# Kernel tuning notes

Measured on AMD Instinct MI355X. Metric: run time of the kernel, lower is better.

The kernel has to match this reference:

```python
import jax, jax.numpy as jnp
import numpy as np

HID = 2048
HEAD = 64
NH = HID // HEAD  # 32 heads
B, T = 4, 2048


def setup_inputs() -> dict:
    key = jax.random.key(0)
    ks = jax.random.split(key, 32)
    def n(i, shape, sc):
        return (jax.random.normal(ks[i], shape, jnp.float32) * sc).astype(jnp.float32)
    return {
        "hidden": n(0, (B, T, HID), 1.0),
        "attn_x": n(1, (B, HID), 1.0),
        "attn_kv": n(2, (B, NH, HEAD, HEAD), 0.1),
        "ffn_x": n(3, (B, HID), 1.0),
        "time_maa_x": n(4, (1, 1, HID), 0.5),
        "time_maa_w": n(5, (1, 1, HID), 0.5),
        "time_maa_k": n(6, (1, 1, HID), 0.5),
        "time_maa_v": n(7, (1, 1, HID), 0.5),
        "time_maa_r": n(8, (1, 1, HID), 0.5),
        "time_maa_g": n(9, (1, 1, HID), 0.5),
        "time_maa_w1": n(10, (HID, 160), 0.02),
        "time_maa_w2": n(11, (5, 32, HID), 0.02),
        "time_decay": n(12, (1, 1, HID), 0.5),
        "time_decay_w1": n(13, (HID, 64), 0.02),
        "time_decay_w2": n(14, (64, HID), 0.02),
        "time_faaaa": n(15, (NH, HEAD), 0.5),
        "receptance_w": n(16, (HID, HID), 0.02),
        "key_w": n(17, (HID, HID), 0.02),
        "value_w": n(18, (HID, HID), 0.02),
        "gate_w": n(19, (HID, HID), 0.02),
        "output_w": n(20, (HID, HID), 0.02),
        "gn_gamma": 1.0 + n(21, (HID,), 0.1),
        "gn_beta": n(22, (HID,), 0.1),
    }


def reference(hidden, attn_x, attn_kv, ffn_x,
              time_maa_x, time_maa_w, time_maa_k, time_maa_v, time_maa_r, time_maa_g,
              time_maa_w1, time_maa_w2, time_decay, time_decay_w1, time_decay_w2,
              time_faaaa, receptance_w, key_w, value_w, gate_w, output_w,
              gn_gamma, gn_beta):
    Bb, Tt, C = hidden.shape
    x = hidden
    shifted = jnp.concatenate([attn_x[:, None, :], x[:, :-1, :]], axis=1)
    dx = shifted - x
    time_mix = x + dx * time_maa_x
    # token-shift LoRA: (B,T,C)@(C,160) -> (5,B*T,32)@(5,32,C) -> five mixes
    xxx = jnp.tanh(time_mix @ time_maa_w1).reshape(Bb * Tt, 5, 32).transpose(1, 0, 2)
    xxx = jnp.einsum('nbk,nkc->nbc', xxx, time_maa_w2)
    mw, mk, mv, mr, mg = xxx.reshape(5, Bb, Tt, C)
    xw = x + dx * (time_maa_w + mw)
    xk = x + dx * (time_maa_k + mk)
    xv = x + dx * (time_maa_v + mv)
    xr = x + dx * (time_maa_r + mr)
    xg = x + dx * (time_maa_g + mg)
    r = (xr @ receptance_w).reshape(Bb, Tt, NH, HEAD).transpose(0, 2, 1, 3)  # (B,H,T,hs)
    k = (xk @ key_w).reshape(Bb, Tt, NH, HEAD).transpose(0, 2, 1, 3)
    v = (xv @ value_w).reshape(Bb, Tt, NH, HEAD).transpose(0, 2, 1, 3)
    g = jax.nn.silu(xg @ gate_w)
    td = time_decay + jnp.tanh(xw @ time_decay_w1) @ time_decay_w2  # (B,T,C)
    w = jnp.exp(-jnp.exp(td)).reshape(Bb, Tt, NH, HEAD).transpose(0, 2, 1, 3)
    # Source updates layer_state only AFTER the time loop, so inside the loop the
    # state is the constant attn_kv:  out_t = r_t @ (u * (k_t v_t^T) + S0).
    rk = jnp.einsum('bhtd,hd,bhtd->bht', r, time_faaaa, k)
    out = rk[..., None] * v + jnp.einsum('bhtd,bhde->bhte', r, attn_kv)  # (B,H,T,hs)
    new_attn_kv = k[:, :, -1, :, None] * v[:, :, -1, None, :] + w[:, :, -1, :, None] * attn_kv
    new_attn_x = hidden[:, -1]
    out = out.transpose(0, 2, 1, 3).reshape(Bb, Tt, C)
    # keras GroupNormalization(groups=NH) on (B,T,C): stats over (T, within-group channels)
    go = out.reshape(Bb, Tt, NH, HEAD)
    mean = go.mean(axis=(1, 3), keepdims=True)
    var = go.var(axis=(1, 3), keepdims=True)
    eps = 1e-5 * HEAD ** 2
    out = ((go - mean) * jax.lax.rsqrt(var + eps)).reshape(Bb, Tt, C) * gn_gamma + gn_beta
    out = (out * g) @ output_w
    return out, new_attn_x, new_attn_kv, ffn_x
```

## Files before the change

kernel.cpp:

```cpp
#include <hip/hip_runtime.h>

#define HID 2048
#define TSEQ 2048
#define BBATCH 4
#define MROWS 8192
#define NHEADS 32

typedef float fvec4 __attribute__((ext_vector_type(4)));
typedef unsigned short usvec4 __attribute__((ext_vector_type(4)));
typedef unsigned short usvec8 __attribute__((ext_vector_type(8)));
typedef __bf16 bh8 __attribute__((ext_vector_type(8)));
typedef float f32x4 __attribute__((ext_vector_type(4)));

__device__ __forceinline__ float bf2f(unsigned short u){
  return __uint_as_float(((unsigned int)u) << 16);
}
__device__ __forceinline__ unsigned short f2bf(float f){
  unsigned int u = __float_as_uint(f);
  return (unsigned short)((u + 0x7fffu + ((u >> 16) & 1u)) >> 16);
}
__device__ __forceinline__ void gll16(const void* g, void* lds){
  __builtin_amdgcn_global_load_lds(
      (const __attribute__((address_space(1))) unsigned int*)g,
      (__attribute__((address_space(3))) unsigned int*)lds, 16, 0, 0);
}

__global__ void tcast_kernel(const float* __restrict__ in, unsigned short* __restrict__ out,
                             int R, int C){
  __shared__ float tile[32][33];
  int c0 = blockIdx.x * 32, r0 = blockIdx.y * 32;
  int tx = threadIdx.x, ty = threadIdx.y;
  for (int i = ty; i < 32; i += 8){
    int r = r0 + i, c = c0 + tx;
    tile[i][tx] = (r < R && c < C) ? in[(size_t)r * C + c] : 0.f;
  }
  __syncthreads();
  for (int i = ty; i < 32; i += 8){
    int c = c0 + i, r = r0 + tx;
    if (c < C && r < R) out[(size_t)c * R + r] = f2bf(tile[tx][i]);
  }
}

__global__ void zero_stats_kernel(float* __restrict__ gsum, float* __restrict__ gsqs){
  int i = threadIdx.x;
  gsum[i] = 0.f;
  gsqs[i] = 0.f;
}

__global__ void tmix_kernel(const float* __restrict__ hidden, const float* __restrict__ attn_x,
                            const float* __restrict__ tmx, unsigned short* __restrict__ tm){
  int i4 = blockIdx.x * 256 + threadIdx.x;
  int row = i4 >> 9;
  int c4 = i4 & 511;
  fvec4 x = *(const fvec4*)&hidden[(size_t)i4 * 4];
  fvec4 p;
  if ((row & (TSEQ - 1)) == 0){
    int b = row >> 11;
    p = *(const fvec4*)&attn_x[b * HID + c4 * 4];
  } else {
    p = *(const fvec4*)&hidden[(size_t)(i4 - 512) * 4];
  }
  fvec4 tx = *(const fvec4*)&tmx[c4 * 4];
  fvec4 t = x + (p - x) * tx;
  usvec4 o;
  o[0]=f2bf(t[0]); o[1]=f2bf(t[1]); o[2]=f2bf(t[2]); o[3]=f2bf(t[3]);
  *(usvec4*)&tm[(size_t)i4 * 4] = o;
}

template<int ACT, int OUTBF16>
__global__ __launch_bounds__(256, 2) void gemm_kernel(
    const unsigned short* __restrict__ A, const unsigned short* __restrict__ Bt,
    void* __restrict__ Cptr, int M, int N, int K, int ldc)
{
  __shared__ unsigned short As[128 * 32];
  __shared__ unsigned short Bs[128 * 32];
  const int tid = threadIdx.x;
  const int lane = tid & 63;
  const int w = tid >> 6;
  const int wr = w >> 1, wc = w & 1;
  const int lr = lane & 15, lq = lane >> 4;
  const int rowBase = blockIdx.y * 128;
  const int colBase = blockIdx.x * 128;

  const int arow = tid >> 2;
  const int ach = tid & 3;
  const unsigned short* aptr0 = A + (size_t)(rowBase + arow) * K + ach * 8;
  const unsigned short* aptr1 = aptr0 + (size_t)64 * K;
  int br0 = colBase + arow;      if (br0 > N - 1) br0 = N - 1;
  int br1 = colBase + arow + 64; if (br1 > N - 1) br1 = N - 1;
  const unsigned short* bptr0 = Bt + (size_t)br0 * K + ach * 8;
  const unsigned short* bptr1 = Bt + (size_t)br1 * K + ach * 8;

  f32x4 acc[4][4] = {};

  const int nk = K >> 5;
  for (int kk = 0; kk < nk; ++kk){
    gll16(aptr0, &As[tid * 8]);
    gll16(aptr1, &As[(tid + 256) * 8]);
    gll16(bptr0, &Bs[tid * 8]);
    gll16(bptr1, &Bs[(tid + 256) * 8]);
    aptr0 += 32; aptr1 += 32; bptr0 += 32; bptr1 += 32;
    __syncthreads();
    bh8 af[4], bfv[4];
    #pragma unroll
    for (int m = 0; m < 4; ++m)
      af[m] = *reinterpret_cast<const bh8*>(&As[(wr * 64 + m * 16 + lr) * 32 + lq * 8]);
    #pragma unroll
    for (int n = 0; n < 4; ++n)
      bfv[n] = *reinterpret_cast<const bh8*>(&Bs[(wc * 64 + n * 16 + lr) * 32 + lq * 8]);
    #pragma unroll
    for (int m = 0; m < 4; ++m)
      #pragma unroll
      for (int n = 0; n < 4; ++n)
        acc[m][n] = __builtin_amdgcn_mfma_f32_16x16x32_bf16(af[m], bfv[n], acc[m][n], 0, 0, 0);
    __syncthreads();
  }

  #pragma unroll
  for (int m = 0; m < 4; ++m){
    int gr0 = rowBase + wr * 64 + m * 16 + lq * 4;
    #pragma unroll
    for (int n = 0; n < 4; ++n){
      int gc = colBase + wc * 64 + n * 16 + lr;
      if (gc < N){
        #pragma unroll
        for (int q = 0; q < 4; ++q){
          float v = acc[m][n][q];
          if constexpr (ACT == 1) v = tanhf(v);
          else if constexpr (ACT == 2) v = v / (1.0f + __expf(-v));
          size_t off = (size_t)(gr0 + q) * ldc + gc;
          if constexpr (OUTBF16) ((unsigned short*)Cptr)[off] = f2bf(v);
          else                   ((float*)Cptr)[off] = v;
        }
      }
    }
  }
}

__global__ __launch_bounds__(256) void mix_kernel(
    const float* __restrict__ xxx, const float* __restrict__ hidden,
    const float* __restrict__ attn_x, const float* __restrict__ w2,
    const float* __restrict__ tmk, const float* __restrict__ tmv,
    const float* __restrict__ tmr, const float* __restrict__ tmg,
    unsigned short* __restrict__ xk, unsigned short* __restrict__ xv,
    unsigned short* __restrict__ xr, unsigned short* __restrict__ xg)
{
  __shared__ __attribute__((aligned(16))) unsigned short smem[20992];
  unsigned short* xs   = smem;
  unsigned short* w2t  = smem + 10752;
  unsigned short* out4 = smem;

  const int tid = threadIdx.x;
  const int r0 = blockIdx.y * 64, c0 = blockIdx.x * 64;
  const int w = tid >> 6, lane = tid & 63, lr = lane & 15, lq = lane >> 4;

  for (int idx = tid; idx < 64 * 40; idx += 256){
    int r = idx / 40, cq = idx - r * 40;
    fvec4 v = *(const fvec4*)&xxx[(size_t)(r0 + r) * 160 + cq * 4];
    usvec4 o;
    o[0]=f2bf(v[0]); o[1]=f2bf(v[1]); o[2]=f2bf(v[2]); o[3]=f2bf(v[3]);
    *(usvec4*)&xs[r * 168 + cq * 4] = o;
  }
  for (int idx = tid; idx < 4 * 32 * 16; idx += 256){
    int n = idx >> 9;
    int rem = idx & 511;
    int j = rem >> 4, cq = rem & 15;
    fvec4 v = *(const fvec4*)&w2[(size_t)((n + 1) * 32 + j) * HID + c0 + cq * 4];
    #pragma unroll
    for (int cc = 0; cc < 4; ++cc)
      w2t[(n * 64 + cq * 4 + cc) * 40 + j] = f2bf(v[cc]);
  }
  __syncthreads();

  f32x4 acc[4][4] = {};
  #pragma unroll
  for (int n = 0; n < 4; ++n){
    bh8 afr = *reinterpret_cast<const bh8*>(&xs[(w * 16 + lr) * 168 + (n + 1) * 32 + lq * 8]);
    #pragma unroll
    for (int ct = 0; ct < 4; ++ct){
      bh8 bfr = *reinterpret_cast<const bh8*>(&w2t[(n * 64 + ct * 16 + lr) * 40 + lq * 8]);
      acc[ct][n] = __builtin_amdgcn_mfma_f32_16x16x32_bf16(afr, bfr, acc[ct][n], 0, 0, 0);
    }
  }
  __syncthreads();

  #pragma unroll
  for (int ct = 0; ct < 4; ++ct){
    int gc = c0 + ct * 16 + lr;
    float tk_ = tmk[gc], tv_ = tmv[gc], tr_ = tmr[gc], tg_ = tmg[gc];
    #pragma unroll
    for (int q = 0; q < 4; ++q){
      int row64 = w * 16 + lq * 4 + q;
      int gr = r0 + row64;
      size_t rowoff = (size_t)gr * HID + gc;
      float xx = hidden[rowoff];
      float pp = ((gr & (TSEQ - 1)) == 0) ? attn_x[(gr >> 11) * HID + gc]
                                          : hidden[rowoff - HID];
      float dxv = pp - xx;
      int lo = row64 * 72 + ct * 16 + lr;
      out4[(0 * 64 * 72) + lo] = f2bf(xx + dxv * (tk_ + acc[ct][0][q]));
      out4[(1 * 64 * 72) + lo] = f2bf(xx + dxv * (tv_ + acc[ct][1][q]));
      out4[(2 * 64 * 72) + lo] = f2bf(xx + dxv * (tr_ + acc[ct][2][q]));
      out4[(3 * 64 * 72) + lo] = f2bf(xx + dxv * (tg_ + acc[ct][3][q]));
    }
  }
  __syncthreads();

  #pragma unroll
  for (int a = 0; a < 4; ++a){
    unsigned short* dst = (a == 0) ? xk : (a == 1) ? xv : (a == 2) ? xr : xg;
    #pragma unroll
    for (int pass = 0; pass < 2; ++pass){
      int row64 = pass * 32 + (tid >> 3);
      int c8 = (tid & 7) * 8;
      usvec8 v8 = *(const usvec8*)&out4[(a * 64 + row64) * 72 + c8];
      *(usvec8*)&dst[(size_t)(r0 + row64) * HID + c0 + c8] = v8;
    }
  }
}

__global__ __launch_bounds__(256) void attn_kernel(
    const unsigned short* __restrict__ rb, const unsigned short* __restrict__ kb,
    const unsigned short* __restrict__ vb, const float* __restrict__ attn_kv,
    const float* __restrict__ faaaa, unsigned short* __restrict__ out0b,
    float* __restrict__ gsum, float* __restrict__ gsqs)
{
  const int bh = blockIdx.y;
  const int b = bh >> 5, h = bh & 31;
  const int tid = threadIdx.x, lane = tid & 63, w = tid >> 6;
  const int lr = lane & 15, lq = lane >> 4;
  const int t0 = blockIdx.x * 256 + w * 64;
  const size_t rowbase = (size_t)(b * TSEQ + t0) * HID + h * 64;

  const float* akvp = attn_kv + (size_t)bh * 4096;
  bh8 bfr[2][4];
  #pragma unroll
  for (int kk = 0; kk < 2; ++kk)
    #pragma unroll
    for (int n = 0; n < 4; ++n)
      #pragma unroll
      for (int j = 0; j < 8; ++j)
        bfr[kk][n][j] = (__bf16)akvp[(kk * 32 + lq * 8 + j) * 64 + n * 16 + lr];

  float fa0[8], fa1[8];
  #pragma unroll
  for (int j = 0; j < 8; ++j){
    fa0[j] = faaaa[h * 64 + lq * 8 + j];
    fa1[j] = faaaa[h * 64 + 32 + lq * 8 + j];
  }

  __shared__ __attribute__((aligned(16))) float rk_s[4][64];
  __shared__ __attribute__((aligned(16))) unsigned short outb[4][64][72];

  f32x4 acc[4][4] = {};
  #pragma unroll
  for (int m = 0; m < 4; ++m){
    size_t ra = rowbase + (size_t)(m * 16 + lr) * HID;
    bh8 a0 = *reinterpret_cast<const bh8*>(&rb[ra + lq * 8]);
    bh8 a1 = *reinterpret_cast<const bh8*>(&rb[ra + 32 + lq * 8]);
    usvec8 k0 = *reinterpret_cast<const usvec8*>(&kb[ra + lq * 8]);
    usvec8 k1 = *reinterpret_cast<const usvec8*>(&kb[ra + 32 + lq * 8]);
    float p = 0.f;
    #pragma unroll
    for (int j = 0; j < 8; ++j){
      p += (float)a0[j] * fa0[j] * bf2f(k0[j]);
      p += (float)a1[j] * fa1[j] * bf2f(k1[j]);
    }
    p += __shfl_xor(p, 16, 64);
    p += __shfl_xor(p, 32, 64);
    if (lq == 0) rk_s[w][m * 16 + lr] = p;
    #pragma unroll
    for (int n = 0; n < 4; ++n){
      acc[m][n] = __builtin_amdgcn_mfma_f32_16x16x32_bf16(a0, bfr[0][n], acc[m][n], 0, 0, 0);
      acc[m][n] = __builtin_amdgcn_mfma_f32_16x16x32_bf16(a1, bfr[1][n], acc[m][n], 0, 0, 0);
    }
  }
  __syncthreads();

  float ssum = 0.f, ssq = 0.f;
  #pragma unroll
  for (int m = 0; m < 4; ++m){
    fvec4 rk4 = *(const fvec4*)&rk_s[w][m * 16 + lq * 4];
    #pragma unroll
    for (int n = 0; n < 4; ++n){
      int col = n * 16 + lr;
      #pragma unroll
      for (int q = 0; q < 4; ++q){
        int row = m * 16 + lq * 4 + q;
        float vv = bf2f(vb[rowbase + (size_t)row * HID + col]);
        float o = acc[m][n][q] + rk4[q] * vv;
        ssum += o; ssq += o * o;
        outb[w][row][col] = f2bf(o);
      }
    }
  }
  __syncthreads();
  #pragma unroll
  for (int pass = 0; pass < 8; ++pass){
    int row = pass * 8 + (lane >> 3);
    int c8 = (lane & 7) * 8;
    usvec8 o8 = *(const usvec8*)&outb[w][row][c8];
    *(usvec8*)&out0b[rowbase + (size_t)row * HID + c8] = o8;
  }
  #pragma unroll
  for (int off2 = 32; off2 > 0; off2 >>= 1){
    ssum += __shfl_xor(ssum, off2, 64);
    ssq  += __shfl_xor(ssq,  off2, 64);
  }
  if (lane == 0){ atomicAdd(&gsum[bh], ssum); atomicAdd(&gsqs[bh], ssq); }
}

__global__ void gn_stats_kernel(const float* __restrict__ gsum, const float* __restrict__ gsqs,
                                float* __restrict__ meaninv){
  int g = threadIdx.x;
  const float n = (float)(TSEQ * 64);
  float mean = gsum[g] / n;
  float var = gsqs[g] / n - mean * mean;
  meaninv[2 * g]     = mean;
  meaninv[2 * g + 1] = rsqrtf(var + 1e-5f * 64.0f * 64.0f);
}

__global__ void ynorm_kernel(const unsigned short* __restrict__ out0b,
                             const unsigned short* __restrict__ gb,
                             const float* __restrict__ meaninv, const float* __restrict__ gamma,
                             const float* __restrict__ beta, unsigned short* __restrict__ yb){
  int i4 = blockIdx.x * 256 + threadIdx.x;
  int row = i4 >> 9, c4 = i4 & 511;
  int b = row >> 11;
  int c = c4 * 4;
  int g = b * 32 + (c >> 6);
  float mean = meaninv[2 * g], inv = meaninv[2 * g + 1];
  usvec4 o4 = *(const usvec4*)&out0b[(size_t)i4 * 4];
  usvec4 gv = *(const usvec4*)&gb[(size_t)i4 * 4];
  fvec4 ga = *(const fvec4*)&gamma[c];
  fvec4 be = *(const fvec4*)&beta[c];
  usvec4 y;
  #pragma unroll
  for (int cc = 0; cc < 4; ++cc){
    float val = ((bf2f(o4[cc]) - mean) * inv * ga[cc] + be[cc]) * bf2f(gv[cc]);
    y[cc] = f2bf(val);
  }
  *(usvec4*)&yb[(size_t)i4 * 4] = y;
}

__global__ void lastrow_mix_kernel(const float* __restrict__ xxx, const float* __restrict__ hidden,
    const float* __restrict__ w2, const float* __restrict__ tmw, const float* __restrict__ tmk,
    const float* __restrict__ tmv, float* __restrict__ xw_l, float* __restrict__ xk_l,
    float* __restrict__ xv_l){
  int b = blockIdx.y;
  int c = blockIdx.x * 256 + threadIdx.x;
  __shared__ float xsr[160];
  int i = b * TSEQ + (TSEQ - 1);
  if (threadIdx.x < 160) xsr[threadIdx.x] = xxx[(size_t)i * 160 + threadIdx.x];
  __syncthreads();
  float mw = 0.f, mk = 0.f, mv = 0.f;
  for (int j = 0; j < 32; ++j){
    mw += xsr[j]      * w2[(size_t)(j)      * HID + c];
    mk += xsr[32 + j] * w2[(size_t)(32 + j) * HID + c];
    mv += xsr[64 + j] * w2[(size_t)(64 + j) * HID + c];
  }
  float x = hidden[(size_t)i * HID + c];
  float prev = hidden[(size_t)(i - 1) * HID + c];
  float dx = prev - x;
  xw_l[b * HID + c] = x + dx * (tmw[c] + mw);
  xk_l[b * HID + c] = x + dx * (tmk[c] + mk);
  xv_l[b * HID + c] = x + dx * (tmv[c] + mv);
}

__global__ void decay1_part_kernel(const float* __restrict__ xw_l, const float* __restrict__ tdw1,
                                   float* __restrict__ dpart){
  int b = blockIdx.y;
  int chunk = blockIdx.x;
  int j = threadIdx.x & 63, sub = threadIdx.x >> 6;
  float s = 0.f;
  int cbase = chunk * 128 + sub * 32;
  for (int r = 0; r < 32; ++r){
    int c = cbase + r;
    s += xw_l[b * HID + c] * tdw1[(size_t)c * 64 + j];
  }
  __shared__ float red[4][64];
  red[sub][j] = s;
  __syncthreads();
  if (sub == 0)
    dpart[((size_t)b * 16 + chunk) * 64 + j] = red[0][j] + red[1][j] + red[2][j] + red[3][j];
}

__global__ void decay1_reduce_kernel(const float* __restrict__ dpart, float* __restrict__ hdec){
  int tid = threadIdx.x;
  int b = tid >> 6, j = tid & 63;
  float s = 0.f;
  #pragma unroll
  for (int chunk = 0; chunk < 16; ++chunk)
    s += dpart[((size_t)b * 16 + chunk) * 64 + j];
  hdec[b * 64 + j] = tanhf(s);
}

__global__ __launch_bounds__(256) void lastrow_kv_part_kernel(
    const float* __restrict__ xk_l, const float* __restrict__ xv_l,
    const float* __restrict__ keyw, const float* __restrict__ valw,
    float* __restrict__ kpart, float* __restrict__ vpart){
  int c = blockIdx.x * 256 + threadIdx.x;
  int chunk = blockIdx.y;
  __shared__ float xs[2][4][128];
  for (int i = threadIdx.x; i < 512; i += 256){
    int b = i >> 7, r = i & 127;
    xs[0][b][r] = xk_l[b * HID + chunk * 128 + r];
    xs[1][b][r] = xv_l[b * HID + chunk * 128 + r];
  }
  __syncthreads();
  float ka[4] = {0,0,0,0}, va[4] = {0,0,0,0};
  for (int r = 0; r < 128; ++r){
    int c2 = chunk * 128 + r;
    float kw = keyw[(size_t)c2 * HID + c];
    float vw = valw[(size_t)c2 * HID + c];
    #pragma unroll
    for (int b = 0; b < 4; ++b){
      ka[b] += xs[0][b][r] * kw;
      va[b] += xs[1][b][r] * vw;
    }
  }
  #pragma unroll
  for (int b = 0; b < 4; ++b){
    kpart[((size_t)chunk * 4 + b) * HID + c] = ka[b];
    vpart[((size_t)chunk * 4 + b) * HID + c] = va[b];
  }
}

__global__ void lastrow_kv_reduce_kernel(
    const float* __restrict__ kpart, const float* __restrict__ vpart,
    const float* __restrict__ hdec, const float* __restrict__ tdw2,
    const float* __restrict__ tdecay, float* __restrict__ klast,
    float* __restrict__ vlast, float* __restrict__ wlast){
  int c = blockIdx.x * 256 + threadIdx.x;
  float ka[4] = {0,0,0,0}, va[4] = {0,0,0,0};
  for (int chunk = 0; chunk < 16; ++chunk){
    #pragma unroll
    for (int b = 0; b < 4; ++b){
      ka[b] += kpart[((size_t)chunk * 4 + b) * HID + c];
      va[b] += vpart[((size_t)chunk * 4 + b) * HID + c];
    }
  }
  float tdc = tdecay[c];
  float td[4] = {tdc, tdc, tdc, tdc};
  for (int j = 0; j < 64; ++j){
    float w2v = tdw2[(size_t)j * HID + c];
    #pragma unroll
    for (int b = 0; b < 4; ++b) td[b] += hdec[b * 64 + j] * w2v;
  }
  #pragma unroll
  for (int b = 0; b < 4; ++b){
    klast[b * HID + c] = ka[b];
    vlast[b * HID + c] = va[b];
    wlast[b * HID + c] = expf(-expf(td[b]));
  }
}

__global__ void newkv_kernel(const float* __restrict__ klast, const float* __restrict__ vlast,
    const float* __restrict__ wlast, const float* __restrict__ attn_kv,
    float* __restrict__ outkv){
  int idx = blockIdx.x * 256 + threadIdx.x;
  int b = idx >> 17;
  int h = (idx >> 12) & 31;
  int d = (idx >> 6) & 63;
  int e = idx & 63;
  float kl = klast[b * HID + h * 64 + d];
  float vl = vlast[b * HID + h * 64 + e];
  float wl = wlast[b * HID + h * 64 + d];
  outkv[idx] = kl * vl + wl * attn_kv[idx];
}

__global__ void copies_kernel(const float* __restrict__ hidden, const float* __restrict__ ffnx,
                              float* __restrict__ out_attnx, float* __restrict__ out_ffnx){
  int i = blockIdx.x * 256 + threadIdx.x;
  if (i < BBATCH * HID){
    int b = i >> 11, c = i & 2047;
    out_attnx[i] = hidden[((size_t)(b * TSEQ + TSEQ - 1)) * HID + c];
    out_ffnx[i] = ffnx[i];
  }
}

extern "C" void kernel_launch(void* const* d_in, const int* in_sizes, int n_in,
                              void* d_out, int out_size, void* d_ws, size_t ws_size,
                              hipStream_t stream)
{
  (void)in_sizes; (void)n_in; (void)out_size;
  const float* hidden = (const float*)d_in[0];
  const float* attn_x = (const float*)d_in[1];
  const float* attn_kv = (const float*)d_in[2];
  const float* ffn_x = (const float*)d_in[3];
  const float* tmaa_x = (const float*)d_in[4];
  const float* tmaa_w = (const float*)d_in[5];
  const float* tmaa_k = (const float*)d_in[6];
  const float* tmaa_v = (const float*)d_in[7];
  const float* tmaa_r = (const float*)d_in[8];
  const float* tmaa_g = (const float*)d_in[9];
  const float* w1 = (const float*)d_in[10];
  const float* w2 = (const float*)d_in[11];
  const float* tdecay = (const float*)d_in[12];
  const float* tdw1 = (const float*)d_in[13];
  const float* tdw2 = (const float*)d_in[14];
  const float* faaaa = (const float*)d_in[15];
  const float* recw = (const float*)d_in[16];
  const float* keyw = (const float*)d_in[17];
  const float* valw = (const float*)d_in[18];
  const float* gatew = (const float*)d_in[19];
  const float* outw = (const float*)d_in[20];
  const float* gamma = (const float*)d_in[21];
  const float* beta = (const float*)d_in[22];

  float* out_main  = (float*)d_out;
  float* out_attnx = out_main + (size_t)16777216;
  float* out_kv    = out_attnx + 8192;
  float* out_ffn   = out_kv + 524288;

  unsigned short* wr_t = (unsigned short*)d_out;
  unsigned short* wk_t = wr_t + (size_t)4194304;
  unsigned short* wv_t = wk_t + (size_t)4194304;
  unsigned short* wg_t = wv_t + (size_t)4194304;
  unsigned short* out0b = (unsigned short*)d_out;

  char* ws = (char*)d_ws;
  size_t off = 0;
  auto alloc = [&](size_t bytes) -> void* {
    void* p = ws + off; off += (bytes + 255) & ~(size_t)255; return p;
  };
  unsigned short* wo_t = (unsigned short*)alloc(2048ull * 2048 * 2);
  unsigned short* w1_t = (unsigned short*)alloc(160ull * 2048 * 2);
  float* xxx           = (float*)alloc((size_t)MROWS * 160 * 4);
  unsigned short* bufA = (unsigned short*)alloc((size_t)MROWS * HID * 2);
  unsigned short* bufB = (unsigned short*)alloc((size_t)MROWS * HID * 2);
  unsigned short* bufC = (unsigned short*)alloc((size_t)MROWS * HID * 2);
  unsigned short* bufD = (unsigned short*)alloc((size_t)MROWS * HID * 2);
  unsigned short* bufE = (unsigned short*)alloc((size_t)MROWS * HID * 2);
  float* gsum    = (float*)alloc(128 * 4);
  float* gsqs    = (float*)alloc(128 * 4);
  float* meaninv = (float*)alloc(256 * 4);
  float* xw_l  = (float*)alloc(BBATCH * HID * 4);
  float* xk_l  = (float*)alloc(BBATCH * HID * 4);
  float* xv_l  = (float*)alloc(BBATCH * HID * 4);
  float* klast = (float*)alloc(BBATCH * HID * 4);
  float* vlast = (float*)alloc(BBATCH * HID * 4);
  float* wlast = (float*)alloc(BBATCH * HID * 4);
  float* hdec  = (float*)alloc(BBATCH * 64 * 4);
  float* kpart = (float*)alloc(16ull * BBATCH * HID * 4);
  float* vpart = (float*)alloc(16ull * BBATCH * HID * 4);
  float* dpart = (float*)alloc((size_t)BBATCH * 16 * 64 * 4);

  if (off > ws_size) return;

  unsigned short* tm = bufA;
  unsigned short* xg = bufA;
  unsigned short* xr = bufB;
  unsigned short* kb = bufB;
  unsigned short* yb = bufB;
  unsigned short* xk = bufC;
  unsigned short* vb = bufC;
  unsigned short* xv = bufD;
  unsigned short* gb = bufD;
  unsigned short* rb = bufE;

  dim3 tb(32, 8);
  tcast_kernel<<<dim3(64, 64), tb, 0, stream>>>(recw,  wr_t, 2048, 2048);
  tcast_kernel<<<dim3(64, 64), tb, 0, stream>>>(keyw,  wk_t, 2048, 2048);
  tcast_kernel<<<dim3(64, 64), tb, 0, stream>>>(valw,  wv_t, 2048, 2048);
  tcast_kernel<<<dim3(64, 64), tb, 0, stream>>>(gatew, wg_t, 2048, 2048);
  tcast_kernel<<<dim3(64, 64), tb, 0, stream>>>(outw,  wo_t, 2048, 2048);
  tcast_kernel<<<dim3(5, 64),  tb, 0, stream>>>(w1,    w1_t, 2048, 160);
  zero_stats_kernel<<<1, 128, 0, stream>>>(gsum, gsqs);

  tmix_kernel<<<16384, 256, 0, stream>>>(hidden, attn_x, tmaa_x, tm);

  gemm_kernel<1, 0><<<dim3(2, 64), 256, 0, stream>>>(tm, w1_t, xxx, MROWS, 160, HID, 160);

  mix_kernel<<<dim3(32, 128), 256, 0, stream>>>(xxx, hidden, attn_x, w2,
      tmaa_k, tmaa_v, tmaa_r, tmaa_g, xk, xv, xr, xg);

  gemm_kernel<0, 1><<<dim3(16, 64), 256, 0, stream>>>(xr, wr_t, rb, MROWS, HID, HID, HID);
  gemm_kernel<0, 1><<<dim3(16, 64), 256, 0, stream>>>(xk, wk_t, kb, MROWS, HID, HID, HID);
  gemm_kernel<0, 1><<<dim3(16, 64), 256, 0, stream>>>(xv, wv_t, vb, MROWS, HID, HID, HID);
  gemm_kernel<2, 1><<<dim3(16, 64), 256, 0, stream>>>(xg, wg_t, gb, MROWS, HID, HID, HID);

  attn_kernel<<<dim3(8, 128), 256, 0, stream>>>(rb, kb, vb, attn_kv, faaaa,
                                                out0b, gsum, gsqs);
  gn_stats_kernel<<<1, 128, 0, stream>>>(gsum, gsqs, meaninv);
  ynorm_kernel<<<16384, 256, 0, stream>>>(out0b, gb, meaninv, gamma, beta, yb);

  gemm_kernel<0, 0><<<dim3(16, 64), 256, 0, stream>>>(yb, wo_t, out_main, MROWS, HID, HID, HID);

  lastrow_mix_kernel<<<dim3(8, 4), 256, 0, stream>>>(xxx, hidden, w2, tmaa_w, tmaa_k, tmaa_v,
                                                     xw_l, xk_l, xv_l);
  decay1_part_kernel<<<dim3(16, 4), 256, 0, stream>>>(xw_l, tdw1, dpart);
  decay1_reduce_kernel<<<1, 256, 0, stream>>>(dpart, hdec);
  lastrow_kv_part_kernel<<<dim3(8, 16), 256, 0, stream>>>(xk_l, xv_l, keyw, valw, kpart, vpart);
  lastrow_kv_reduce_kernel<<<8, 256, 0, stream>>>(kpart, vpart, hdec, tdw2, tdecay,
                                                  klast, vlast, wlast);
  newkv_kernel<<<2048, 256, 0, stream>>>(klast, vlast, wlast, attn_kv, out_kv);
  copies_kernel<<<32, 256, 0, stream>>>(hidden, ffn_x, out_attnx, out_ffn);
}
```

Before: 777.3 us.

## Add 256x256-tile double-buffered bf16 MFMA GEMM for the large projections

Adds a new GEMM kernel with 256x256 output tiles, 512 threads (8 waves, each computing 128x64), and a double-buffered LDS pipeline. Each stage is loaded with direct global-to-LDS copies using an XOR-swizzled layout. It replaces the 128x128-tile GEMM for the r/k/v/g and output projections, raising arithmetic intensity and cutting global traffic per FLOP. The cost is 128KB of LDS per block, which may limit occupancy. The grid also shrinks to 256 blocks, which may underfill the GPU's CUs.

```diff
diff --git a/kernel.cpp b/kernel.cpp
--- a/kernel.cpp
+++ b/kernel.cpp
@@ -132,6 +132,113 @@
           if constexpr (OUTBF16) ((unsigned short*)Cptr)[off] = f2bf(v);
           else                   ((float*)Cptr)[off] = v;
         }
+      }
+    }
+  }
+}
+
+template<int ACT, int OUTBF16>
+__global__ __launch_bounds__(512, 2) void gemm256_kernel(
+    const unsigned short* __restrict__ A, const unsigned short* __restrict__ Bt,
+    void* __restrict__ Cptr, int K)
+{
+  __shared__ unsigned short smem[65536];
+  const int tid = threadIdx.x;
+  const int lane = tid & 63, w = tid >> 6;
+  const int wr = w >> 2, wc = w & 3;
+  const int lr = lane & 15, lq = lane >> 4;
+  const int rowBase = blockIdx.y * 256;
+  const int colBase = blockIdx.x * 256;
+  const int N = gridDim.x * 256;
+
+  const unsigned short* srcp[8];
+  int dstoff[8];
+  #pragma unroll
+  for (int l = 0; l < 8; ++l){
+    int ci = (l & 3) * 512 + tid;
+    int r = ci >> 3, c = ci & 7;
+    int gchunk = c ^ (r & 7);
+    const unsigned short* base = (l < 4) ? A : Bt;
+    int grow = ((l < 4) ? rowBase : colBase) + r;
+    srcp[l] = base + (size_t)grow * K + gchunk * 8;
+    dstoff[l] = ((l < 4) ? 0 : 16384) + ci * 8;
+  }
+
+  f32x4 acc[8][4] = {};
+
+  auto STAGE = [&](unsigned short* buf){
+    #pragma unroll
+    for (int l = 0; l < 8; ++l){
+      gll16(srcp[l], buf + dstoff[l]);
+      srcp[l] += 64;
+    }
+  };
+
+  auto COMPUTE = [&](const unsigned short* buf){
+    const unsigned short* aB = buf;
+    const unsigned short* bB = buf + 16384;
+    #pragma unroll
+    for (int mh = 0; mh < 2; ++mh){
+      #pragma unroll
+      for (int nh = 0; nh < 2; ++nh){
+        bh8 af[4][2], bf[2][2];
+        #pragma unroll
+        for (int m2 = 0; m2 < 4; ++m2){
+          int row = wr * 128 + (mh * 4 + m2) * 16 + lr;
+          #pragma unroll
+          for (int s = 0; s < 2; ++s)
+            af[m2][s] = *reinterpret_cast<const bh8*>(
+                &aB[row * 64 + (((s * 4 + lq) ^ (row & 7)) * 8)]);
+        }
+        #pragma unroll
+        for (int n2 = 0; n2 < 2; ++n2){
+          int row = wc * 64 + (nh * 2 + n2) * 16 + lr;
+          #pragma unroll
+          for (int s = 0; s < 2; ++s)
+            bf[n2][s] = *reinterpret_cast<const bh8*>(
+                &bB[row * 64 + (((s * 4 + lq) ^ (row & 7)) * 8)]);
+        }
+        #pragma unroll
+        for (int m2 = 0; m2 < 4; ++m2)
+          #pragma unroll
+          for (int n2 = 0; n2 < 2; ++n2)
+            #pragma unroll
+            for (int s = 0; s < 2; ++s)
+              acc[mh * 4 + m2][nh * 2 + n2] = __builtin_amdgcn_mfma_f32_16x16x32_bf16(
+                  af[m2][s], bf[n2][s], acc[mh * 4 + m2][nh * 2 + n2], 0, 0, 0);
+      }
+    }
+  };
+
+  unsigned short* buf0 = smem;
+  unsigned short* buf1 = smem + 32768;
+
+  STAGE(buf0);
+  __syncthreads();
+  const int nt = K >> 6;
+  for (int t = 0; t < nt - 1; ++t){
+    unsigned short* cur = (t & 1) ? buf1 : buf0;
+    unsigned short* nxt = (t & 1) ? buf0 : buf1;
+    STAGE(nxt);
+    COMPUTE(cur);
+    __syncthreads();
+  }
+  COMPUTE((nt & 1) ? buf0 : buf1);
+
+  #pragma unroll
+  for (int m = 0; m < 8; ++m){
+    int gr0 = rowBase + wr * 128 + m * 16 + lq * 4;
+    #pragma unroll
+    for (int n = 0; n < 4; ++n){
+      int gc = colBase + wc * 64 + n * 16 + lr;
+      #pragma unroll
+      for (int q = 0; q < 4; ++q){
+        float v = acc[m][n][q];
+        if constexpr (ACT == 1) v = tanhf(v);
+        else if constexpr (ACT == 2) v = v / (1.0f + __expf(-v));
+        size_t off = (size_t)(gr0 + q) * N + gc;
+        if constexpr (OUTBF16) ((unsigned short*)Cptr)[off] = f2bf(v);
+        else                   ((float*)Cptr)[off] = v;
       }
     }
   }
@@ -575,17 +682,17 @@
   mix_kernel<<<dim3(32, 128), 256, 0, stream>>>(xxx, hidden, attn_x, w2,
       tmaa_k, tmaa_v, tmaa_r, tmaa_g, xk, xv, xr, xg);
 
-  gemm_kernel<0, 1><<<dim3(16, 64), 256, 0, stream>>>(xr, wr_t, rb, MROWS, HID, HID, HID);
-  gemm_kernel<0, 1><<<dim3(16, 64), 256, 0, stream>>>(xk, wk_t, kb, MROWS, HID, HID, HID);
-  gemm_kernel<0, 1><<<dim3(16, 64), 256, 0, stream>>>(xv, wv_t, vb, MROWS, HID, HID, HID);
-  gemm_kernel<2, 1><<<dim3(16, 64), 256, 0, stream>>>(xg, wg_t, gb, MROWS, HID, HID, HID);
+  gemm256_kernel<0, 1><<<dim3(8, 32), 512, 0, stream>>>(xr, wr_t, rb, HID);
+  gemm256_kernel<0, 1><<<dim3(8, 32), 512, 0, stream>>>(xk, wk_t, kb, HID);
+  gemm256_kernel<0, 1><<<dim3(8, 32), 512, 0, stream>>>(xv, wv_t, vb, HID);
+  gemm256_kernel<2, 1><<<dim3(8, 32), 512, 0, stream>>>(xg, wg_t, gb, HID);
 
   attn_kernel<<<dim3(8, 128), 256, 0, stream>>>(rb, kb, vb, attn_kv, faaaa,
                                                 out0b, gsum, gsqs);
   gn_stats_kernel<<<1, 128, 0, stream>>>(gsum, gsqs, meaninv);
   ynorm_kernel<<<16384, 256, 0, stream>>>(out0b, gb, meaninv, gamma, beta, yb);
 
-  gemm_kernel<0, 0><<<dim3(16, 64), 256, 0, stream>>>(yb, wo_t, out_main, MROWS, HID, HID, HID);
+  gemm256_kernel<0, 0><<<dim3(8, 32), 512, 0, stream>>>(yb, wo_t, out_main, HID);
 
   lastrow_mix_kernel<<<dim3(8, 4), 256, 0, stream>>>(xxx, hidden, w2, tmaa_w, tmaa_k, tmaa_v,
                                                      xw_l, xk_l, xv_l);
```

Measured after the change: 699.6 us. 10.0% less time.
